# Kernel optimization log

Measured on AMD Instinct MI355X. Metric: run time of the kernel, lower is better.

The kernel has to match this reference:

```python
import jax, jax.numpy as jnp
import numpy as np

N = 100000   # nodes
E = 1600000  # edges
IN = 512     # in_channels
H = 256      # hidden_channels
C = 40       # out_channels
BITS = 8     # INT8 fake quantization


def fake_quant(x, bits=BITS):
    """Symmetric per-tensor quantize-dequantize with straight-through estimator."""
    qmax = float(2 ** (bits - 1) - 1)
    scale = jnp.max(jnp.abs(x)) / qmax + 1e-12
    q = jnp.clip(jnp.round(x / scale), -qmax - 1.0, qmax) * scale
    # STE: forward = q, backward = identity
    return x + jax.lax.stop_gradient(q - x)


def quant_linear(x, w, b):
    # LinearQuantized: fake-quant inputs and weights, fp accumulate
    return fake_quant(x) @ fake_quant(w).T + b


def gcn_propagate(x, edge_index):
    """Symmetric-normalized sparse propagation: out = D^-1/2 A D^-1/2 x."""
    src, dst = edge_index[0], edge_index[1]
    deg = jax.ops.segment_sum(jnp.ones((E,), x.dtype), dst, num_segments=N)
    dinv = jnp.where(deg > 0, jax.lax.rsqrt(jnp.maximum(deg, 1.0)), 0.0)
    coef = dinv[src] * dinv[dst]                     # [E]
    msgs = x[src] * coef[:, None]                    # [E, C]
    return jax.ops.segment_sum(msgs, dst, num_segments=N)  # [N, C]


def setup_inputs() -> dict:
    key = jax.random.key(0)
    ks = jax.random.split(key, 6)
    x = jax.random.normal(ks[0], (N, IN), jnp.float32)
    edge_index = jax.random.randint(ks[1], (2, E), 0, N, dtype=jnp.int32)
    w1 = jax.random.normal(ks[2], (H, IN), jnp.float32) * (1.0 / np.sqrt(IN))
    b1 = jnp.zeros((H,), jnp.float32)
    w2 = jax.random.normal(ks[3], (C, H), jnp.float32) * (1.0 / np.sqrt(H))
    b2 = jnp.zeros((C,), jnp.float32)
    return {"x": x, "edge_index": edge_index, "w1": w1, "b1": b1, "w2": w2, "b2": b2}


def reference(x, edge_index, w1, b1, w2, b2):
    # dropout: identity in eval mode
    h = jax.nn.relu(quant_linear(x, w1, b1))         # [N, H]
    z = quant_linear(h, w2, b2)                      # [N, C]
    z = gcn_propagate(z, edge_index)                 # [N, C]
    return jax.nn.log_softmax(z, axis=1)
```

## Files before the change

### kernel.cpp

```cpp
#include <hip/hip_runtime.h>
#include <hip/hip_bf16.h>
#include <stdint.h>
#include <stddef.h>

#define NN   100000
#define NE   1600000
#define INC  512
#define HID  256
#define OC   40
#define OCP  48

#define LDK  72
#define LDB2 264

#define NBKT ((NN + 255) / 256)

typedef __bf16 bf16_t;
typedef __bf16 bf16x8 __attribute__((ext_vector_type(8)));
typedef __bf16 bf16x4 __attribute__((ext_vector_type(4)));
typedef float  f32x4  __attribute__((ext_vector_type(4)));

__device__ unsigned g_amax_bits[4];
__device__ float    g_dinv[NN];
__device__ bf16_t   g_qw1[HID * INC];
__device__ bf16_t   g_qw2[OCP * HID];
__device__ float    g_h[(size_t)NN * HID];
__device__ float    g_z[(size_t)NN * OC];
__device__ unsigned g_chist[NBKT];
__device__ unsigned g_cstart[NBKT + 1];
__device__ unsigned g_ccur[NBKT];
__device__ uint2    g_bin[NE];
__device__ unsigned g_rowstart[NN + 1];
__device__ int      g_csr_src[NE];

__device__ __forceinline__ bf16_t quant1(float v, float rs) {
    return (bf16_t)fminf(fmaxf(rintf(v * rs), -128.0f), 127.0f);
}

__global__ void init_kernel() {
    int idx = blockIdx.x * blockDim.x + threadIdx.x;
    int stride = gridDim.x * blockDim.x;
    for (int i = idx; i < NBKT; i += stride) g_chist[i] = 0u;
    for (int i = idx; i < OCP * HID; i += stride) g_qw2[i] = (bf16_t)0.0f;
    if (idx < 4) g_amax_bits[idx] = 0u;
}

__global__ void chist_kernel(const int* __restrict__ ei) {
    const int* dst = ei + NE;
    __shared__ unsigned hist[NBKT];
    int t = threadIdx.x;
    for (int i = t; i < NBKT; i += 256) hist[i] = 0u;
    __syncthreads();
    int idx = blockIdx.x * 256 + t;
    int stride = gridDim.x * 256;
    for (int e = idx; e < NE; e += stride) atomicAdd(&hist[dst[e] >> 8], 1u);
    __syncthreads();
    for (int i = t; i < NBKT; i += 256) {
        unsigned c = hist[i];
        if (c) atomicAdd(&g_chist[i], c);
    }
}

__global__ void cscan_kernel() {
    int t = threadIdx.x;
    unsigned v = (t < NBKT) ? g_chist[t] : 0u;
    int lane = t & 63, wv = t >> 6;
    unsigned sc = v;
#pragma unroll
    for (int off = 1; off < 64; off <<= 1) {
        unsigned n = __shfl_up(sc, off, 64);
        if (lane >= off) sc += n;
    }
    __shared__ unsigned ws[8];
    if (lane == 63) ws[wv] = sc;
    __syncthreads();
    unsigned woff = 0;
    for (int w = 0; w < 8; w++) if (w < wv) woff += ws[w];
    unsigned excl = woff + sc - v;
    if (t < NBKT) { g_cstart[t] = excl; g_ccur[t] = excl; }
    if (t == 0) g_cstart[NBKT] = NE;
}

#define BIN_BLOCKS 200
#define BIN_EPB    (NE / BIN_BLOCKS)
__global__ void bin_kernel(const int* __restrict__ ei) {
    const int* srcp = ei;
    const int* dstp = ei + NE;
    __shared__ unsigned hist[NBKT];
    __shared__ unsigned base[NBKT];
    int t = threadIdx.x;
    int e0 = blockIdx.x * BIN_EPB, e1 = e0 + BIN_EPB;
    for (int i = t; i < NBKT; i += 256) hist[i] = 0u;
    __syncthreads();
    for (int e = e0 + t; e < e1; e += 256) atomicAdd(&hist[dstp[e] >> 8], 1u);
    __syncthreads();
    for (int i = t; i < NBKT; i += 256) {
        unsigned c = hist[i];
        base[i] = c ? atomicAdd(&g_ccur[i], c) : 0u;
        hist[i] = 0u;
    }
    __syncthreads();
    for (int e = e0 + t; e < e1; e += 256) {
        int d = dstp[e], s = srcp[e];
        int b = d >> 8;
        unsigned r = atomicAdd(&hist[b], 1u);
        g_bin[base[b] + r] = make_uint2((unsigned)s, (unsigned)d);
    }
}

__global__ void local_kernel() {
    int b = blockIdx.x, t = threadIdx.x;
    unsigned e0 = g_cstart[b], e1 = g_cstart[b + 1];
    __shared__ unsigned hist[256];
    __shared__ unsigned curs[256];
    __shared__ unsigned wsum[4];
    hist[t] = 0u;
    __syncthreads();
    for (unsigned e = e0 + t; e < e1; e += 256) atomicAdd(&hist[g_bin[e].y & 255], 1u);
    __syncthreads();
    unsigned v = hist[t];
    int lane = t & 63, wv = t >> 6;
    unsigned sc = v;
#pragma unroll
    for (int off = 1; off < 64; off <<= 1) {
        unsigned n = __shfl_up(sc, off, 64);
        if (lane >= off) sc += n;
    }
    if (lane == 63) wsum[wv] = sc;
    __syncthreads();
    unsigned woff = 0;
    for (int w = 0; w < 4; w++) if (w < wv) woff += wsum[w];
    unsigned excl = woff + sc - v;
    int node = b * 256 + t;
    if (node < NN) {
        g_rowstart[node] = e0 + excl;
        g_dinv[node] = v ? rsqrtf((float)v) : 0.0f;
    }
    if (b == 0 && t == 0) g_rowstart[NN] = NE;
    curs[t] = excl;
    __syncthreads();
    for (unsigned e = e0 + t; e < e1; e += 256) {
        uint2 ed = g_bin[e];
        unsigned r = atomicAdd(&curs[ed.y & 255], 1u);
        g_csr_src[e0 + r] = (int)ed.x;
    }
}

__global__ void absmax_kernel(const float* __restrict__ src, int n4, int slot) {
    int idx = blockIdx.x * blockDim.x + threadIdx.x;
    int stride = gridDim.x * blockDim.x;
    const f32x4* s4 = (const f32x4*)src;
    float m = 0.0f;
    for (int i = idx; i < n4; i += stride) {
        f32x4 v = s4[i];
        m = fmaxf(m, fmaxf(fmaxf(fabsf(v.x), fabsf(v.y)),
                           fmaxf(fabsf(v.z), fabsf(v.w))));
    }
#pragma unroll
    for (int off = 32; off > 0; off >>= 1) m = fmaxf(m, __shfl_xor(m, off, 64));
    __shared__ float sm[4];
    if ((threadIdx.x & 63) == 0) sm[threadIdx.x >> 6] = m;
    __syncthreads();
    if (threadIdx.x == 0) {
        float mm = fmaxf(fmaxf(sm[0], sm[1]), fmaxf(sm[2], sm[3]));
        atomicMax(&g_amax_bits[slot], __float_as_uint(mm));
    }
}

__global__ void quantw_kernel(const float* __restrict__ src, int n4, int slot, int which) {
    bf16_t* dst = which ? g_qw2 : g_qw1;
    float rs = 1.0f / (__uint_as_float(g_amax_bits[slot]) / 127.0f + 1e-12f);
    int idx = blockIdx.x * blockDim.x + threadIdx.x;
    int stride = gridDim.x * blockDim.x;
    const f32x4* s4 = (const f32x4*)src;
    bf16x4* d4 = (bf16x4*)dst;
    for (int i = idx; i < n4; i += stride) {
        f32x4 v = s4[i];
        bf16x4 o;
        o[0] = quant1(v.x, rs); o[1] = quant1(v.y, rs);
        o[2] = quant1(v.z, rs); o[3] = quant1(v.w, rs);
        d4[i] = o;
    }
}

__launch_bounds__(256)
__global__ void gemm1_kernel(const float* __restrict__ x, const float* __restrict__ b1) {
    __shared__ bf16_t lA[2][128 * LDK];
    __shared__ bf16_t lB[2][128 * LDK];
    int t = threadIdx.x;
    int mtile = blockIdx.x >> 1, ntile = blockIdx.x & 1;
    int lane = t & 63, wv = t >> 6;
    int quad = lane >> 4, l16 = lane & 15;
    int mq = wv >> 1, nq = wv & 1;

    float scale_x = __uint_as_float(g_amax_bits[0]) / 127.0f + 1e-12f;
    float rs = 1.0f / scale_x;

    int srow = t >> 3;
    int sch  = t & 7;

    const float*  xbase[4];
    const bf16_t* wbase[4];
#pragma unroll
    for (int p = 0; p < 4; p++) {
        int gr = mtile * 128 + p * 32 + srow; if (gr >= NN) gr = NN - 1;
        xbase[p] = x + (size_t)gr * INC + sch * 8;
        wbase[p] = g_qw1 + (size_t)(ntile * 128 + p * 32 + srow) * INC + sch * 8;
    }

    f32x4 av[4][2]; bf16x8 bv[4];
#pragma unroll
    for (int p = 0; p < 4; p++) {
        av[p][0] = *(const f32x4*)(xbase[p]);
        av[p][1] = *(const f32x4*)(xbase[p] + 4);
        bv[p]    = *(const bf16x8*)(wbase[p]);
    }

    f32x4 acc[4][4] = {};
#pragma unroll 1
    for (int kit = 0; kit < 8; kit++) {
        int bs = kit & 1;
#pragma unroll
        for (int p = 0; p < 4; p++) {
            int row = p * 32 + srow;
            bf16x8 o;
            o[0] = quant1(av[p][0].x, rs); o[1] = quant1(av[p][0].y, rs);
            o[2] = quant1(av[p][0].z, rs); o[3] = quant1(av[p][0].w, rs);
            o[4] = quant1(av[p][1].x, rs); o[5] = quant1(av[p][1].y, rs);
            o[6] = quant1(av[p][1].z, rs); o[7] = quant1(av[p][1].w, rs);
            *(bf16x8*)(lA[bs] + row * LDK + sch * 8) = o;
            *(bf16x8*)(lB[bs] + row * LDK + sch * 8) = bv[p];
        }
        if (kit + 1 < 8) {
#pragma unroll
            for (int p = 0; p < 4; p++) {
                av[p][0] = *(const f32x4*)(xbase[p] + (kit + 1) * 64);
                av[p][1] = *(const f32x4*)(xbase[p] + (kit + 1) * 64 + 4);
                bv[p]    = *(const bf16x8*)(wbase[p] + (kit + 1) * 64);
            }
        }
        __syncthreads();
#pragma unroll
        for (int k32 = 0; k32 < 2; k32++) {
            int cs = (k32 * 4 + quad) * 8;
            bf16x8 a[4], b[4];
#pragma unroll
            for (int i = 0; i < 4; i++)
                a[i] = *(const bf16x8*)(lA[bs] + (mq * 64 + i * 16 + l16) * LDK + cs);
#pragma unroll
            for (int j = 0; j < 4; j++)
                b[j] = *(const bf16x8*)(lB[bs] + (nq * 64 + j * 16 + l16) * LDK + cs);
#pragma unroll
            for (int i = 0; i < 4; i++)
#pragma unroll
                for (int j = 0; j < 4; j++)
                    acc[i][j] = __builtin_amdgcn_mfma_f32_16x16x32_bf16(a[i], b[j], acc[i][j], 0, 0, 0);
        }
    }
    float s = scale_x * (__uint_as_float(g_amax_bits[1]) / 127.0f + 1e-12f);
    float lmax = 0.0f;
#pragma unroll
    for (int j = 0; j < 4; j++) {
        int col = ntile * 128 + nq * 64 + j * 16 + l16;
        float bias = b1[col];
#pragma unroll
        for (int i = 0; i < 4; i++) {
#pragma unroll
            for (int r = 0; r < 4; r++) {
                int grow = mtile * 128 + mq * 64 + i * 16 + quad * 4 + r;
                float v = fmaxf(s * acc[i][j][r] + bias, 0.0f);
                lmax = fmaxf(lmax, v);
                if (grow < NN) g_h[(size_t)grow * HID + col] = v;
            }
        }
    }
#pragma unroll
    for (int off = 32; off > 0; off >>= 1) lmax = fmaxf(lmax, __shfl_xor(lmax, off, 64));
    if (lane == 0) atomicMax(&g_amax_bits[3], __float_as_uint(lmax));
}

__launch_bounds__(256)
__global__ void gemm2_kernel(const float* __restrict__ b2) {
    __shared__ bf16_t lB2[OCP * LDB2];
    __shared__ bf16_t lA2[128 * LDK];
    int t = threadIdx.x;
    int mtile = blockIdx.x;
    int lane = t & 63, wv = t >> 6;
    int quad = lane >> 4, l16 = lane & 15;

#pragma unroll
    for (int p = 0; p < 6; p++) {
        int ci = p * 256 + t;
        int row = ci >> 5, ch = ci & 31;
        *(bf16x8*)(lB2 + row * LDB2 + ch * 8) =
            *(const bf16x8*)(g_qw2 + row * 256 + ch * 8);
    }

    float scale_h = __uint_as_float(g_amax_bits[3]) / 127.0f + 1e-12f;
    float rs = 1.0f / scale_h;
    int srow = t >> 3, sch = t & 7;
    const float* hbase[4];
#pragma unroll
    for (int p = 0; p < 4; p++) {
        int gr = mtile * 128 + p * 32 + srow; if (gr >= NN) gr = NN - 1;
        hbase[p] = g_h + (size_t)gr * HID + sch * 8;
    }

    f32x4 acc[2][3] = {};
#pragma unroll 1
    for (int kit = 0; kit < 4; kit++) {
        if (kit) __syncthreads();
#pragma unroll
        for (int p = 0; p < 4; p++) {
            int row = p * 32 + srow;
            f32x4 v0 = *(const f32x4*)(hbase[p] + kit * 64);
            f32x4 v1 = *(const f32x4*)(hbase[p] + kit * 64 + 4);
            bf16x8 o;
            o[0] = quant1(v0.x, rs); o[1] = quant1(v0.y, rs);
            o[2] = quant1(v0.z, rs); o[3] = quant1(v0.w, rs);
            o[4] = quant1(v1.x, rs); o[5] = quant1(v1.y, rs);
            o[6] = quant1(v1.z, rs); o[7] = quant1(v1.w, rs);
            *(bf16x8*)(lA2 + row * LDK + sch * 8) = o;
        }
        __syncthreads();
#pragma unroll
        for (int k32 = 0; k32 < 2; k32++) {
            int csA = (k32 * 4 + quad) * 8;
            int chB = (kit * 8 + k32 * 4 + quad) * 8;
            bf16x8 a[2], b[3];
#pragma unroll
            for (int i = 0; i < 2; i++)
                a[i] = *(const bf16x8*)(lA2 + (wv * 32 + i * 16 + l16) * LDK + csA);
#pragma unroll
            for (int j = 0; j < 3; j++)
                b[j] = *(const bf16x8*)(lB2 + (j * 16 + l16) * LDB2 + chB);
#pragma unroll
            for (int i = 0; i < 2; i++)
#pragma unroll
                for (int j = 0; j < 3; j++)
                    acc[i][j] = __builtin_amdgcn_mfma_f32_16x16x32_bf16(a[i], b[j], acc[i][j], 0, 0, 0);
        }
    }
    float s = scale_h * (__uint_as_float(g_amax_bits[2]) / 127.0f + 1e-12f);
#pragma unroll
    for (int j = 0; j < 3; j++) {
        int col = j * 16 + l16;
        float bias = (col < OC) ? b2[col] : 0.0f;
#pragma unroll
        for (int i = 0; i < 2; i++) {
#pragma unroll
            for (int r = 0; r < 4; r++) {
                int grow = mtile * 128 + wv * 32 + i * 16 + quad * 4 + r;
                if (col < OC && grow < NN)
                    g_z[(size_t)grow * OC + col] = s * acc[i][j][r] + bias;
            }
        }
    }
}

__launch_bounds__(256)
__global__ void gather_kernel(float* __restrict__ out) {
    int node = (blockIdx.x * 256 + threadIdx.x) >> 6;
    int lane = threadIdx.x & 63;
    if (node >= NN) return;
    unsigned e0 = g_rowstart[node], e1 = g_rowstart[node + 1];
    float dinvd = g_dinv[node];
    float acc = 0.0f;
    unsigned e = e0;
    for (; e + 2 <= e1; e += 2) {
        int s0 = g_csr_src[e], s1 = g_csr_src[e + 1];
        float c0 = g_dinv[s0] * dinvd;
        float c1 = g_dinv[s1] * dinvd;
        float z0 = (lane < OC) ? g_z[(size_t)s0 * OC + lane] : 0.0f;
        float z1 = (lane < OC) ? g_z[(size_t)s1 * OC + lane] : 0.0f;
        acc += z0 * c0 + z1 * c1;
    }
    if (e < e1) {
        int s0 = g_csr_src[e];
        float c0 = g_dinv[s0] * dinvd;
        float z0 = (lane < OC) ? g_z[(size_t)s0 * OC + lane] : 0.0f;
        acc += z0 * c0;
    }
    float m = (lane < OC) ? acc : -1e30f;
#pragma unroll
    for (int off = 32; off > 0; off >>= 1) m = fmaxf(m, __shfl_xor(m, off, 64));
    float ex = (lane < OC) ? __expf(acc - m) : 0.0f;
    float ssum = ex;
#pragma unroll
    for (int off = 32; off > 0; off >>= 1) ssum += __shfl_xor(ssum, off, 64);
    float lg = __logf(ssum);
    if (lane < OC) out[(size_t)node * OC + lane] = acc - m - lg;
}

extern "C" void kernel_launch(void* const* d_in, const int* in_sizes, int n_in,
                              void* d_out, int out_size, void* d_ws, size_t ws_size,
                              hipStream_t stream) {
    const float* x  = (const float*)d_in[0];
    const int*   ei = (const int*)d_in[1];
    const float* w1 = (const float*)d_in[2];
    const float* b1 = (const float*)d_in[3];
    const float* w2 = (const float*)d_in[4];
    const float* b2 = (const float*)d_in[5];
    float* out = (float*)d_out;
    (void)d_ws; (void)ws_size; (void)in_sizes; (void)n_in; (void)out_size;

    init_kernel<<<1024, 256, 0, stream>>>();
    chist_kernel<<<128, 256, 0, stream>>>(ei);
    cscan_kernel<<<1, 512, 0, stream>>>();
    bin_kernel<<<BIN_BLOCKS, 256, 0, stream>>>(ei);
    local_kernel<<<NBKT, 256, 0, stream>>>();
    absmax_kernel<<<2048, 256, 0, stream>>>(x,  (NN * INC) / 4, 0);
    absmax_kernel<<<128, 256, 0, stream>>>(w1, (HID * INC) / 4, 1);
    absmax_kernel<<<10, 256, 0, stream>>>(w2,  (OC * HID) / 4, 2);
    quantw_kernel<<<128, 256, 0, stream>>>(w1, (HID * INC) / 4, 1, 0);
    quantw_kernel<<<10, 256, 0, stream>>>(w2,  (OC * HID) / 4, 2, 1);
    gemm1_kernel<<<((NN + 127) / 128) * 2, 256, 0, stream>>>(x, b1);
    gemm2_kernel<<<(NN + 127) / 128, 256, 0, stream>>>(b2);
    gather_kernel<<<(NN + 3) / 4, 256, 0, stream>>>(out);
}
```

Baseline: 634.8 us.

## Switch GEMMs to int8 MFMA with a separate x pre-quantization pass

Both quantized GEMMs now use int8 operands with the i32 16x16x64 i8 MFMA instead of bf16. The input x is quantized once by a new kernel into an int8 buffer, so gemm1 streams int8 rather than fp32 and no longer quantizes inside its loop. This costs an extra full read of x plus a 51MB write and read-back. The gather kernel is unrolled by four with the destination normalization factored out, and two edge-binning kernels get larger grids.

Result: faster. 606.3 us (-4.5%).

```diff
diff --git a/kernel.cpp b/kernel.cpp
--- a/kernel.cpp
+++ b/kernel.cpp
@@ -10,20 +10,19 @@
 #define OC   40
 #define OCP  48
 
-#define LDK  72
-#define LDB2 264
+#define LDS1 144
+#define LDSB2 272
 
 #define NBKT ((NN + 255) / 256)
 
-typedef __bf16 bf16_t;
-typedef __bf16 bf16x8 __attribute__((ext_vector_type(8)));
-typedef __bf16 bf16x4 __attribute__((ext_vector_type(4)));
 typedef float  f32x4  __attribute__((ext_vector_type(4)));
+typedef int    i32x4  __attribute__((ext_vector_type(4)));
 
 __device__ unsigned g_amax_bits[4];
 __device__ float    g_dinv[NN];
-__device__ bf16_t   g_qw1[HID * INC];
-__device__ bf16_t   g_qw2[OCP * HID];
+__device__ signed char g_qx[(size_t)NN * INC];
+__device__ signed char g_qw1[HID * INC];
+__device__ signed char g_qw2[OCP * HID];
 __device__ float    g_h[(size_t)NN * HID];
 __device__ float    g_z[(size_t)NN * OC];
 __device__ unsigned g_chist[NBKT];
@@ -33,15 +32,20 @@
 __device__ unsigned g_rowstart[NN + 1];
 __device__ int      g_csr_src[NE];
 
-__device__ __forceinline__ bf16_t quant1(float v, float rs) {
-    return (bf16_t)fminf(fmaxf(rintf(v * rs), -128.0f), 127.0f);
+__device__ __forceinline__ float quantf(float v, float rs) {
+    return fminf(fmaxf(rintf(v * rs), -128.0f), 127.0f);
+}
+__device__ __forceinline__ int pack4(float a, float b, float c, float d, float rs) {
+    int q0 = (int)quantf(a, rs), q1 = (int)quantf(b, rs);
+    int q2 = (int)quantf(c, rs), q3 = (int)quantf(d, rs);
+    return (q0 & 255) | ((q1 & 255) << 8) | ((q2 & 255) << 16) | ((q3 & 255) << 24);
 }
 
 __global__ void init_kernel() {
     int idx = blockIdx.x * blockDim.x + threadIdx.x;
     int stride = gridDim.x * blockDim.x;
     for (int i = idx; i < NBKT; i += stride) g_chist[i] = 0u;
-    for (int i = idx; i < OCP * HID; i += stride) g_qw2[i] = (bf16_t)0.0f;
+    for (int i = idx; i < (OCP * HID) / 4; i += stride) ((int*)g_qw2)[i] = 0;
     if (idx < 4) g_amax_bits[idx] = 0u;
 }
 
@@ -81,7 +85,7 @@
     if (t == 0) g_cstart[NBKT] = NE;
 }
 
-#define BIN_BLOCKS 200
+#define BIN_BLOCKS 400
 #define BIN_EPB    (NE / BIN_BLOCKS)
 __global__ void bin_kernel(const int* __restrict__ ei) {
     const int* srcp = ei;
@@ -167,97 +171,100 @@
     }
 }
 
-__global__ void quantw_kernel(const float* __restrict__ src, int n4, int slot, int which) {
-    bf16_t* dst = which ? g_qw2 : g_qw1;
+__global__ void quantx_kernel(const float* __restrict__ src, int n16) {
+    float rs = 1.0f / (__uint_as_float(g_amax_bits[0]) / 127.0f + 1e-12f);
+    int idx = blockIdx.x * blockDim.x + threadIdx.x;
+    int stride = gridDim.x * blockDim.x;
+    i32x4* d = (i32x4*)g_qx;
+    for (int i = idx; i < n16; i += stride) {
+        const f32x4* s = (const f32x4*)(src + (size_t)i * 16);
+        f32x4 v0 = s[0], v1 = s[1], v2 = s[2], v3 = s[3];
+        i32x4 o;
+        o[0] = pack4(v0.x, v0.y, v0.z, v0.w, rs);
+        o[1] = pack4(v1.x, v1.y, v1.z, v1.w, rs);
+        o[2] = pack4(v2.x, v2.y, v2.z, v2.w, rs);
+        o[3] = pack4(v3.x, v3.y, v3.z, v3.w, rs);
+        d[i] = o;
+    }
+}
+
+__global__ void quantw8_kernel(const float* __restrict__ src, int nint, int slot, int which) {
+    int* dst = which ? (int*)g_qw2 : (int*)g_qw1;
     float rs = 1.0f / (__uint_as_float(g_amax_bits[slot]) / 127.0f + 1e-12f);
     int idx = blockIdx.x * blockDim.x + threadIdx.x;
     int stride = gridDim.x * blockDim.x;
-    const f32x4* s4 = (const f32x4*)src;
-    bf16x4* d4 = (bf16x4*)dst;
-    for (int i = idx; i < n4; i += stride) {
-        f32x4 v = s4[i];
-        bf16x4 o;
-        o[0] = quant1(v.x, rs); o[1] = quant1(v.y, rs);
-        o[2] = quant1(v.z, rs); o[3] = quant1(v.w, rs);
-        d4[i] = o;
+    for (int i = idx; i < nint; i += stride) {
+        f32x4 v = *(const f32x4*)(src + (size_t)i * 4);
+        dst[i] = pack4(v.x, v.y, v.z, v.w, rs);
     }
 }
 
 __launch_bounds__(256)
-__global__ void gemm1_kernel(const float* __restrict__ x, const float* __restrict__ b1) {
-    __shared__ bf16_t lA[2][128 * LDK];
-    __shared__ bf16_t lB[2][128 * LDK];
+__global__ void gemm1_kernel(const float* __restrict__ b1) {
+    __shared__ char lA[2][128 * LDS1];
+    __shared__ char lB[2][128 * LDS1];
     int t = threadIdx.x;
     int mtile = blockIdx.x >> 1, ntile = blockIdx.x & 1;
     int lane = t & 63, wv = t >> 6;
     int quad = lane >> 4, l16 = lane & 15;
     int mq = wv >> 1, nq = wv & 1;
 
-    float scale_x = __uint_as_float(g_amax_bits[0]) / 127.0f + 1e-12f;
-    float rs = 1.0f / scale_x;
-
     int srow = t >> 3;
     int sch  = t & 7;
 
-    const float*  xbase[4];
-    const bf16_t* wbase[4];
+    const signed char* xb[4];
+    const signed char* wb[4];
 #pragma unroll
     for (int p = 0; p < 4; p++) {
         int gr = mtile * 128 + p * 32 + srow; if (gr >= NN) gr = NN - 1;
-        xbase[p] = x + (size_t)gr * INC + sch * 8;
-        wbase[p] = g_qw1 + (size_t)(ntile * 128 + p * 32 + srow) * INC + sch * 8;
-    }
-
-    f32x4 av[4][2]; bf16x8 bv[4];
+        xb[p] = g_qx + (size_t)gr * INC + sch * 16;
+        wb[p] = g_qw1 + (size_t)(ntile * 128 + p * 32 + srow) * INC + sch * 16;
+    }
+
+    i32x4 av[4], bv[4];
 #pragma unroll
     for (int p = 0; p < 4; p++) {
-        av[p][0] = *(const f32x4*)(xbase[p]);
-        av[p][1] = *(const f32x4*)(xbase[p] + 4);
-        bv[p]    = *(const bf16x8*)(wbase[p]);
-    }
-
-    f32x4 acc[4][4] = {};
+        av[p] = *(const i32x4*)(xb[p]);
+        bv[p] = *(const i32x4*)(wb[p]);
+    }
+
+    i32x4 acc[4][4] = {};
 #pragma unroll 1
-    for (int kit = 0; kit < 8; kit++) {
+    for (int kit = 0; kit < 4; kit++) {
         int bs = kit & 1;
 #pragma unroll
         for (int p = 0; p < 4; p++) {
             int row = p * 32 + srow;
-            bf16x8 o;
-            o[0] = quant1(av[p][0].x, rs); o[1] = quant1(av[p][0].y, rs);
-            o[2] = quant1(av[p][0].z, rs); o[3] = quant1(av[p][0].w, rs);
-            o[4] = quant1(av[p][1].x, rs); o[5] = quant1(av[p][1].y, rs);
-            o[6] = quant1(av[p][1].z, rs); o[7] = quant1(av[p][1].w, rs);
-            *(bf16x8*)(lA[bs] + row * LDK + sch * 8) = o;
-            *(bf16x8*)(lB[bs] + row * LDK + sch * 8) = bv[p];
-        }
-        if (kit + 1 < 8) {
+            *(i32x4*)(lA[bs] + row * LDS1 + sch * 16) = av[p];
+            *(i32x4*)(lB[bs] + row * LDS1 + sch * 16) = bv[p];
+        }
+        if (kit + 1 < 4) {
 #pragma unroll
             for (int p = 0; p < 4; p++) {
-                av[p][0] = *(const f32x4*)(xbase[p] + (kit + 1) * 64);
-                av[p][1] = *(const f32x4*)(xbase[p] + (kit + 1) * 64 + 4);
-                bv[p]    = *(const bf16x8*)(wbase[p] + (kit + 1) * 64);
+                av[p] = *(const i32x4*)(xb[p] + (kit + 1) * 128);
+                bv[p] = *(const i32x4*)(wb[p] + (kit + 1) * 128);
             }
         }
         __syncthreads();
 #pragma unroll
-        for (int k32 = 0; k32 < 2; k32++) {
-            int cs = (k32 * 4 + quad) * 8;
-            bf16x8 a[4], b[4];
+        for (int ks = 0; ks < 2; ks++) {
+            int cs = ks * 64 + quad * 16;
+            i32x4 a[4], b[4];
 #pragma unroll
             for (int i = 0; i < 4; i++)
-                a[i] = *(const bf16x8*)(lA[bs] + (mq * 64 + i * 16 + l16) * LDK + cs);
+                a[i] = *(const i32x4*)(lA[bs] + (mq * 64 + i * 16 + l16) * LDS1 + cs);
 #pragma unroll
             for (int j = 0; j < 4; j++)
-                b[j] = *(const bf16x8*)(lB[bs] + (nq * 64 + j * 16 + l16) * LDK + cs);
+                b[j] = *(const i32x4*)(lB[bs] + (nq * 64 + j * 16 + l16) * LDS1 + cs);
 #pragma unroll
             for (int i = 0; i < 4; i++)
 #pragma unroll
                 for (int j = 0; j < 4; j++)
-                    acc[i][j] = __builtin_amdgcn_mfma_f32_16x16x32_bf16(a[i], b[j], acc[i][j], 0, 0, 0);
-        }
-    }
-    float s = scale_x * (__uint_as_float(g_amax_bits[1]) / 127.0f + 1e-12f);
+                    acc[i][j] = __builtin_amdgcn_mfma_i32_16x16x64_i8(a[i], b[j], acc[i][j], 0, 0, 0);
+        }
+    }
+    float s = (__uint_as_float(g_amax_bits[0]) / 127.0f + 1e-12f)
+            * (__uint_as_float(g_amax_bits[1]) / 127.0f + 1e-12f);
     float lmax = 0.0f;
 #pragma unroll
     for (int j = 0; j < 4; j++) {
@@ -268,7 +275,7 @@
 #pragma unroll
             for (int r = 0; r < 4; r++) {
                 int grow = mtile * 128 + mq * 64 + i * 16 + quad * 4 + r;
-                float v = fmaxf(s * acc[i][j][r] + bias, 0.0f);
+                float v = fmaxf(s * (float)acc[i][j][r] + bias, 0.0f);
                 lmax = fmaxf(lmax, v);
                 if (grow < NN) g_h[(size_t)grow * HID + col] = v;
             }
@@ -281,19 +288,19 @@
 
 __launch_bounds__(256)
 __global__ void gemm2_kernel(const float* __restrict__ b2) {
-    __shared__ bf16_t lB2[OCP * LDB2];
-    __shared__ bf16_t lA2[128 * LDK];
+    __shared__ char lB2[OCP * LDSB2];
+    __shared__ char lA2[128 * LDS1];
     int t = threadIdx.x;
     int mtile = blockIdx.x;
     int lane = t & 63, wv = t >> 6;
     int quad = lane >> 4, l16 = lane & 15;
 
 #pragma unroll
-    for (int p = 0; p < 6; p++) {
+    for (int p = 0; p < 3; p++) {
         int ci = p * 256 + t;
-        int row = ci >> 5, ch = ci & 31;
-        *(bf16x8*)(lB2 + row * LDB2 + ch * 8) =
-            *(const bf16x8*)(g_qw2 + row * 256 + ch * 8);
+        int row = ci >> 4, ch = ci & 15;
+        *(i32x4*)(lB2 + row * LDSB2 + ch * 16) =
+            *(const i32x4*)(g_qw2 + row * 256 + ch * 16);
     }
 
     float scale_h = __uint_as_float(g_amax_bits[3]) / 127.0f + 1e-12f;
@@ -303,42 +310,44 @@
 #pragma unroll
     for (int p = 0; p < 4; p++) {
         int gr = mtile * 128 + p * 32 + srow; if (gr >= NN) gr = NN - 1;
-        hbase[p] = g_h + (size_t)gr * HID + sch * 8;
-    }
-
-    f32x4 acc[2][3] = {};
+        hbase[p] = g_h + (size_t)gr * HID + sch * 16;
+    }
+
+    i32x4 acc[2][3] = {};
 #pragma unroll 1
-    for (int kit = 0; kit < 4; kit++) {
+    for (int kit = 0; kit < 2; kit++) {
         if (kit) __syncthreads();
 #pragma unroll
         for (int p = 0; p < 4; p++) {
             int row = p * 32 + srow;
-            f32x4 v0 = *(const f32x4*)(hbase[p] + kit * 64);
-            f32x4 v1 = *(const f32x4*)(hbase[p] + kit * 64 + 4);
-            bf16x8 o;
-            o[0] = quant1(v0.x, rs); o[1] = quant1(v0.y, rs);
-            o[2] = quant1(v0.z, rs); o[3] = quant1(v0.w, rs);
-            o[4] = quant1(v1.x, rs); o[5] = quant1(v1.y, rs);
-            o[6] = quant1(v1.z, rs); o[7] = quant1(v1.w, rs);
-            *(bf16x8*)(lA2 + row * LDK + sch * 8) = o;
+            const float* hp = hbase[p] + kit * 128;
+            f32x4 v0 = *(const f32x4*)(hp);
+            f32x4 v1 = *(const f32x4*)(hp + 4);
+            f32x4 v2 = *(const f32x4*)(hp + 8);
+            f32x4 v3 = *(const f32x4*)(hp + 12);
+            i32x4 o;
+            o[0] = pack4(v0.x, v0.y, v0.z, v0.w, rs);
+            o[1] = pack4(v1.x, v1.y, v1.z, v1.w, rs);
+            o[2] = pack4(v2.x, v2.y, v2.z, v2.w, rs);
+            o[3] = pack4(v3.x, v3.y, v3.z, v3.w, rs);
+            *(i32x4*)(lA2 + row * LDS1 + sch * 16) = o;
         }
         __syncthreads();
 #pragma unroll
-        for (int k32 = 0; k32 < 2; k32++) {
-            int csA = (k32 * 4 + quad) * 8;
-            int chB = (kit * 8 + k32 * 4 + quad) * 8;
-            bf16x8 a[2], b[3];
+        for (int ks = 0; ks < 2; ks++) {
+            int cs = ks * 64 + quad * 16;
+            i32x4 a[2], b[3];
 #pragma unroll
             for (int i = 0; i < 2; i++)
-                a[i] = *(const bf16x8*)(lA2 + (wv * 32 + i * 16 + l16) * LDK + csA);
+                a[i] = *(const i32x4*)(lA2 + (wv * 32 + i * 16 + l16) * LDS1 + cs);
 #pragma unroll
             for (int j = 0; j < 3; j++)
-                b[j] = *(const bf16x8*)(lB2 + (j * 16 + l16) * LDB2 + chB);
+                b[j] = *(const i32x4*)(lB2 + (j * 16 + l16) * LDSB2 + kit * 128 + cs);
 #pragma unroll
             for (int i = 0; i < 2; i++)
 #pragma unroll
                 for (int j = 0; j < 3; j++)
-                    acc[i][j] = __builtin_amdgcn_mfma_f32_16x16x32_bf16(a[i], b[j], acc[i][j], 0, 0, 0);
+                    acc[i][j] = __builtin_amdgcn_mfma_i32_16x16x64_i8(a[i], b[j], acc[i][j], 0, 0, 0);
         }
     }
     float s = scale_h * (__uint_as_float(g_amax_bits[2]) / 127.0f + 1e-12f);
@@ -352,7 +361,7 @@
             for (int r = 0; r < 4; r++) {
                 int grow = mtile * 128 + wv * 32 + i * 16 + quad * 4 + r;
                 if (col < OC && grow < NN)
-                    g_z[(size_t)grow * OC + col] = s * acc[i][j][r] + bias;
+                    g_z[(size_t)grow * OC + col] = s * (float)acc[i][j][r] + bias;
             }
         }
     }
@@ -367,20 +376,22 @@
     float dinvd = g_dinv[node];
     float acc = 0.0f;
     unsigned e = e0;
-    for (; e + 2 <= e1; e += 2) {
-        int s0 = g_csr_src[e], s1 = g_csr_src[e + 1];
-        float c0 = g_dinv[s0] * dinvd;
-        float c1 = g_dinv[s1] * dinvd;
+    for (; e + 4 <= e1; e += 4) {
+        int s0 = g_csr_src[e],     s1 = g_csr_src[e + 1];
+        int s2 = g_csr_src[e + 2], s3 = g_csr_src[e + 3];
+        float c0 = g_dinv[s0], c1 = g_dinv[s1], c2 = g_dinv[s2], c3 = g_dinv[s3];
         float z0 = (lane < OC) ? g_z[(size_t)s0 * OC + lane] : 0.0f;
         float z1 = (lane < OC) ? g_z[(size_t)s1 * OC + lane] : 0.0f;
-        acc += z0 * c0 + z1 * c1;
-    }
-    if (e < e1) {
+        float z2 = (lane < OC) ? g_z[(size_t)s2 * OC + lane] : 0.0f;
+        float z3 = (lane < OC) ? g_z[(size_t)s3 * OC + lane] : 0.0f;
+        acc += (z0 * c0 + z1 * c1) + (z2 * c2 + z3 * c3);
+    }
+    for (; e < e1; e++) {
         int s0 = g_csr_src[e];
-        float c0 = g_dinv[s0] * dinvd;
         float z0 = (lane < OC) ? g_z[(size_t)s0 * OC + lane] : 0.0f;
-        acc += z0 * c0;
-    }
+        acc += z0 * g_dinv[s0];
+    }
+    acc *= dinvd;
     float m = (lane < OC) ? acc : -1e30f;
 #pragma unroll
     for (int off = 32; off > 0; off >>= 1) m = fmaxf(m, __shfl_xor(m, off, 64));
@@ -405,16 +416,17 @@
     (void)d_ws; (void)ws_size; (void)in_sizes; (void)n_in; (void)out_size;
 
     init_kernel<<<1024, 256, 0, stream>>>();
-    chist_kernel<<<128, 256, 0, stream>>>(ei);
+    chist_kernel<<<256, 256, 0, stream>>>(ei);
     cscan_kernel<<<1, 512, 0, stream>>>();
     bin_kernel<<<BIN_BLOCKS, 256, 0, stream>>>(ei);
     local_kernel<<<NBKT, 256, 0, stream>>>();
     absmax_kernel<<<2048, 256, 0, stream>>>(x,  (NN * INC) / 4, 0);
     absmax_kernel<<<128, 256, 0, stream>>>(w1, (HID * INC) / 4, 1);
     absmax_kernel<<<10, 256, 0, stream>>>(w2,  (OC * HID) / 4, 2);
-    quantw_kernel<<<128, 256, 0, stream>>>(w1, (HID * INC) / 4, 1, 0);
-    quantw_kernel<<<10, 256, 0, stream>>>(w2,  (OC * HID) / 4, 2, 1);
-    gemm1_kernel<<<((NN + 127) / 128) * 2, 256, 0, stream>>>(x, b1);
+    quantx_kernel<<<3200, 256, 0, stream>>>(x, (NN * INC) / 16);
+    quantw8_kernel<<<128, 256, 0, stream>>>(w1, (HID * INC) / 4, 1, 0);
+    quantw8_kernel<<<10, 256, 0, stream>>>(w2,  (OC * HID) / 4, 2, 1);
+    gemm1_kernel<<<((NN + 127) / 128) * 2, 256, 0, stream>>>(b1);
     gemm2_kernel<<<(NN + 127) / 128, 256, 0, stream>>>(b2);
     gather_kernel<<<(NN + 3) / 4, 256, 0, stream>>>(out);
 }
```
